# Optimization experiments

Measured on AMD Instinct MI355X. Metric: run time of the kernel, lower is better.

Reference implementation:

```python
import jax, jax.numpy as jnp
import numpy as np

B, S, H, D = 4, 4096, 8, 128
EPS = 1e-6


def layernorm(x, g, b, axes):
    m = jnp.mean(x, axis=axes, keepdims=True)
    v = jnp.mean(jnp.square(x - m), axis=axes, keepdims=True)
    return (x - m) / jnp.sqrt(v + EPS) * g + b


def setup_inputs() -> dict:
    key = jax.random.key(0)
    ks = jax.random.split(key, 6)
    scale = 0.05
    return {
        "heads_input": jax.random.normal(ks[0], (B, S, H, D), jnp.float32),
        # GroupLinear trans_hid: per-head (2D -> 3D)
        "W_hid": jax.random.normal(ks[1], (H, 2 * D, 3 * D), jnp.float32) * scale,
        "b_hid": jax.random.normal(ks[2], (H, 3 * D), jnp.float32) * scale,
        # GroupLinear trans_og: per-head (2D -> D)
        "W_og": jax.random.normal(ks[3], (H, 2 * D, D), jnp.float32) * scale,
        "b_og": jax.random.normal(ks[4], (H, D), jnp.float32) * scale,
        # LayerNorm affine params (elementwise_affine=True)
        "ln_csum_g": jnp.ones((H, D), jnp.float32),
        "ln_csum_b": jnp.zeros((H, D), jnp.float32),
        "ln_hid_g": jnp.ones((H, 3, D), jnp.float32),
        "ln_hid_b": jnp.zeros((H, 3, D), jnp.float32),
        "ln_og_g": jnp.ones((H, D), jnp.float32),
        "ln_og_b": jnp.zeros((H, D), jnp.float32),
        "init_cx": jnp.zeros((1, H, D), jnp.float32),
    }


def reference(heads_input, W_hid, b_hid, W_og, b_og, ln_csum_g, ln_csum_b,
              ln_hid_g, ln_hid_b, ln_og_g, ln_og_b, init_cx):
    b, s, h, d = heads_input.shape
    # shifted cumulative sum over time, then LayerNorm over (head, dim)
    shifted = jnp.concatenate(
        [jnp.zeros((b, 1, h, d), heads_input.dtype), heads_input[:, :-1]], axis=1)
    csum = layernorm(jnp.cumsum(shifted, axis=1), ln_csum_g, ln_csum_b, (-2, -1))
    cat = jnp.concatenate([heads_input, csum], axis=-1)        # [b,s,h,2d]
    hid = jnp.einsum('bshi,hio->bsho', cat, W_hid) + b_hid     # [b,s,h,3d]
    hid = layernorm(hid.reshape(b, s, h, 3, d), ln_hid_g, ln_hid_b, (-3, -2, -1))
    igate, fgate, hidden = hid[..., 0, :], hid[..., 1, :], hid[..., 2, :]
    fgate = jax.nn.sigmoid(fgate)
    igh = jax.nn.sigmoid(igate) * jax.nn.relu(hidden)
    # LGateFunc: cell_t = fgate_t * cell_{t-1} + igh_t, cell_0 = init_cx
    c0 = jnp.broadcast_to(init_cx, (b, h, d)).astype(heads_input.dtype)
    def step(c, fi):
        f, i = fi
        c = f * c + i
        return c, c
    _, cells = jax.lax.scan(step, c0,
                            (fgate.transpose(1, 0, 2, 3), igh.transpose(1, 0, 2, 3)))
    cell = cells.transpose(1, 0, 2, 3)                          # [b,s,h,d]
    og_in = jnp.concatenate([heads_input, cell], axis=-1)       # [b,s,h,2d]
    og = layernorm(jnp.einsum('bshi,hio->bsho', og_in, W_og) + b_og,
                   ln_og_g, ln_og_b, (-2, -1))
    return jax.nn.sigmoid(og) * cell
```

## Files before the change

kernel.cpp:

```cpp
#include <hip/hip_runtime.h>

#define EPSF 1e-6f


typedef __attribute__((ext_vector_type(8))) short short8v;
typedef __attribute__((ext_vector_type(4))) float float4v;

__device__ __forceinline__ float sigm(float x) { return 1.0f / (1.0f + __expf(-x)); }

__device__ __forceinline__ unsigned short f2bf(float f) {
    unsigned int u = __float_as_uint(f);
    u = (u + 0x7fffu + ((u >> 16) & 1u)) >> 16;
    return (unsigned short)u;
}
__device__ __forceinline__ float bf2f(unsigned short s) { return __uint_as_float(((unsigned int)s) << 16); }
__device__ __forceinline__ float bf2f_lo(unsigned int p) { return __uint_as_float(p << 16); }
__device__ __forceinline__ float bf2f_hi(unsigned int p) { return __uint_as_float(p & 0xffff0000u); }
__device__ __forceinline__ unsigned int pack2bf(float a, float b) {
    return (unsigned int)f2bf(a) | ((unsigned int)f2bf(b) << 16);
}

__device__ __forceinline__ void block_reduce2(float& a, float& b) {
#pragma unroll
    for (int off = 32; off > 0; off >>= 1) {
        a += __shfl_down(a, off);
        b += __shfl_down(b, off);
    }
    __shared__ float sa[8], sb[8];
    int wid = threadIdx.x >> 6;
    int lane = threadIdx.x & 63;
    if (lane == 0) { sa[wid] = a; sb[wid] = b; }
    __syncthreads();
    a = sa[0] + sa[1] + sa[2] + sa[3];
    b = sb[0] + sb[1] + sb[2] + sb[3];
}

__global__ __launch_bounds__(256) void k_prep_w(const float* __restrict__ Wh, const float* __restrict__ Wo,
                                                unsigned short* __restrict__ WTH,
                                                unsigned short* __restrict__ WTO) {
    int idx = blockIdx.x * 256 + threadIdx.x;
    if (idx < 786432) {
        int k = idx & 255;
        int rest = idx >> 8;
        int o = rest % 384;
        int h = rest / 384;
        WTH[idx] = f2bf(Wh[((size_t)h * 256 + k) * 384 + o]);
    } else {
        int i2 = idx - 786432;
        int k = i2 & 255;
        int rest = i2 >> 8;
        int o = rest & 127;
        int h = rest >> 7;
        WTO[i2] = f2bf(Wo[((size_t)h * 256 + k) * 128 + o]);
    }
}

__global__ __launch_bounds__(256) void k_cumsum_a(const float* __restrict__ X, float* __restrict__ cS,
                                                  unsigned short* __restrict__ XB) {
    int t = blockIdx.x * 256 + threadIdx.x;
    int d = t & 127, h = (t >> 7) & 7, k = (t >> 10) & 63, b = t >> 16;
    size_t xbase = (((size_t)(b * 4096 + k * 64)) * 8 + h) * 128 + d;
    size_t pbase = ((size_t)h * 16384 + b * 4096 + k * 64) * 128 + d;
    float s = 0.f;
    for (int j = 0; j < 64; ++j) {
        unsigned short xb = f2bf(X[xbase + (size_t)j * 1024]);
        XB[pbase + (size_t)j * 128] = xb;
        s += bf2f(xb);
    }
    cS[(size_t)((b * 8 + h) * 128 + d) * 64 + k] = s;
}

__global__ __launch_bounds__(256) void k_cumsum_b(const float* __restrict__ cS, float* __restrict__ cO) {
    int wave = (blockIdx.x * 256 + threadIdx.x) >> 6;
    int lane = threadIdx.x & 63;
    size_t idx = (size_t)wave * 64 + lane;
    float v = cS[idx];
    float incl = v;
#pragma unroll
    for (int d = 1; d < 64; d <<= 1) {
        float t = __shfl_up(incl, d);
        if (lane >= d) incl += t;
    }
    cO[idx] = incl - v;
}

__global__ __launch_bounds__(256) void k_cumsum_c(const unsigned short* __restrict__ XB,
                                                  const float* __restrict__ cO,
                                                  unsigned short* __restrict__ CSUMB) {
    int t = blockIdx.x * 256 + threadIdx.x;
    int d = t & 127, h = (t >> 7) & 7, k = (t >> 10) & 63, b = t >> 16;
    int ch = (b * 8 + h) * 128 + d;
    float run = cO[(size_t)ch * 64 + k];
    size_t pbase = ((size_t)h * 16384 + b * 4096 + k * 64) * 128 + d;
    for (int j = 0; j < 64; ++j) {
        float x = bf2f(XB[pbase + (size_t)j * 128]);
        CSUMB[pbase + (size_t)j * 128] = f2bf(run);
        run += x;
    }
}

__global__ __launch_bounds__(256) void k_ln_csum(const unsigned short* __restrict__ CSUMB,
                                                 unsigned short* __restrict__ CSB,
                                                 const float* __restrict__ g, const float* __restrict__ bb) {
    int bs = blockIdx.x, t = threadIdx.x;
    int h = t >> 5, c = t & 31;
    size_t u2i = ((size_t)h * 16384 + bs) * 32 + c;
    uint2 u = ((const uint2*)CSUMB)[u2i];
    float4 v;
    v.x = bf2f_lo(u.x); v.y = bf2f_hi(u.x);
    v.z = bf2f_lo(u.y); v.w = bf2f_hi(u.y);
    float s = v.x + v.y + v.z + v.w;
    float ss = v.x * v.x + v.y * v.y + v.z * v.z + v.w * v.w;
    block_reduce2(s, ss);
    float m = s * (1.f / 1024.f);
    float var = ss * (1.f / 1024.f) - m * m;
    float r = rsqrtf(fmaxf(var, 0.f) + EPSF);
    float4 gv = ((const float4*)g)[t];
    float4 bv = ((const float4*)bb)[t];
    uint2 o;
    o.x = pack2bf((v.x - m) * r * gv.x + bv.x, (v.y - m) * r * gv.y + bv.y);
    o.y = pack2bf((v.z - m) * r * gv.z + bv.z, (v.w - m) * r * gv.w + bv.w);
    ((uint2*)CSB)[u2i] = o;
}

__global__ __launch_bounds__(512) void k_gemm_bf16(const unsigned short* __restrict__ A1,
                                                   const unsigned short* __restrict__ A2,
                                                   const unsigned short* __restrict__ Wt,
                                                   const float* __restrict__ bias,
                                                   unsigned short* __restrict__ OUT, int Nw, int m0,
                                                   int nbx) {
    __shared__ short As[2][8192];
    __shared__ short Bs[2][8192];
    int bid = blockIdx.x;
    int h = bid & 7;
    int rest = bid >> 3;
    int bx = rest % nbx;
    int by = rest / nbx;
    int t0 = threadIdx.x;
    int lane = t0 & 63, wid = t0 >> 6;
    int wr = wid >> 1, wc = wid & 1;
    int l15 = lane & 15, l4 = lane >> 4;
    int lr = lane >> 3, lc = lane & 7;
    const int bxc = bx * 128;
    const size_t mbase = (size_t)(m0 + by * 128);
    const size_t aplane = (size_t)h * 16384;

    float4v acc[2][4];
#pragma unroll
    for (int i = 0; i < 2; ++i)
#pragma unroll
        for (int j = 0; j < 4; ++j) acc[i][j] = (float4v)(0.f);

    auto STAGE = [&](int t, int buf) {
        const unsigned short* src = (t < 2) ? A1 : A2;
        int kofs = (t & 1) * 64;
#pragma unroll
        for (int it = 0; it < 2; ++it) {
            int r0 = wid * 16 + it * 8;
            int r = r0 + lr;
            int c = lc ^ (r & 7);
            size_t g = (aplane + mbase + r) * 128 + kofs + c * 8;
            __builtin_amdgcn_global_load_lds((const __attribute__((address_space(1))) void*)(src + g),
                                             (__attribute__((address_space(3))) void*)(&As[buf][r0 * 64]),
                                             16, 0, 0);
        }
#pragma unroll
        for (int it = 0; it < 2; ++it) {
            int n0 = wid * 16 + it * 8;
            int cl = n0 + lr;
            int c = lc ^ (cl & 7);
            size_t g = ((size_t)(h * Nw + bxc + cl)) * 256 + t * 64 + c * 8;
            __builtin_amdgcn_global_load_lds((const __attribute__((address_space(1))) void*)(Wt + g),
                                             (__attribute__((address_space(3))) void*)(&Bs[buf][n0 * 64]),
                                             16, 0, 0);
        }
    };

    STAGE(0, 0);
#pragma unroll
    for (int t = 0; t < 4; ++t) {
        int cur = t & 1;
        if (t < 3) {
            STAGE(t + 1, cur ^ 1);
            asm volatile("s_waitcnt vmcnt(4)" ::: "memory");
        } else {
            asm volatile("s_waitcnt vmcnt(0)" ::: "memory");
        }
        __builtin_amdgcn_s_barrier();
        __builtin_amdgcn_sched_barrier(0);
#pragma unroll
        for (int kk = 0; kk < 2; ++kk) {
            short8v a[2], b[4];
#pragma unroll
            for (int i = 0; i < 2; ++i) {
                int r = wr * 32 + i * 16 + l15;
                int slot = (kk * 4 + l4) ^ (r & 7);
                a[i] = *(const short8v*)(&As[cur][r * 64 + slot * 8]);
            }
#pragma unroll
            for (int j = 0; j < 4; ++j) {
                int c = wc * 64 + j * 16 + l15;
                int slot = (kk * 4 + l4) ^ (c & 7);
                b[j] = *(const short8v*)(&Bs[cur][c * 64 + slot * 8]);
            }
#pragma unroll
            for (int i = 0; i < 2; ++i)
#pragma unroll
                for (int j = 0; j < 4; ++j)
                    acc[i][j] = __builtin_amdgcn_mfma_f32_16x16x32_bf16(a[i], b[j], acc[i][j], 0, 0, 0);
        }
        __builtin_amdgcn_sched_barrier(0);
        __builtin_amdgcn_s_barrier();
    }
#pragma unroll
    for (int j = 0; j < 4; ++j) {
        int o = bxc + wc * 64 + j * 16 + l15;
        float bv = bias[h * Nw + o];
#pragma unroll
        for (int i = 0; i < 2; ++i) {
            int mlb = by * 128 + wr * 32 + i * 16 + l4 * 4;
#pragma unroll
            for (int q = 0; q < 4; ++q) {
                OUT[((size_t)(mlb + q) * 8 + h) * Nw + o] = f2bf(acc[i][j][q] + bv);
            }
        }
    }
}

__global__ __launch_bounds__(256) void k_ln_gates(const unsigned short* __restrict__ HID,
                                                  unsigned short* __restrict__ FG,
                                                  unsigned short* __restrict__ IG,
                                                  const float* __restrict__ g, const float* __restrict__ bb,
                                                  int m0) {
    __shared__ float sm[3072];
    int bsl = blockIdx.x, t = threadIdx.x;
    int bs = m0 + bsl;
    const uint4* row = (const uint4*)(HID + (size_t)bsl * 3072);
    float s = 0.f, ss = 0.f;
    for (int idx = t; idx < 384; idx += 256) {
        uint4 u = row[idx];
        float f0 = bf2f_lo(u.x), f1 = bf2f_hi(u.x);
        float f2 = bf2f_lo(u.y), f3 = bf2f_hi(u.y);
        float f4 = bf2f_lo(u.z), f5 = bf2f_hi(u.z);
        float f6 = bf2f_lo(u.w), f7 = bf2f_hi(u.w);
        float* p = sm + idx * 8;
        p[0] = f0; p[1] = f1; p[2] = f2; p[3] = f3; p[4] = f4; p[5] = f5; p[6] = f6; p[7] = f7;
        s += f0 + f1 + f2 + f3 + f4 + f5 + f6 + f7;
        ss += f0 * f0 + f1 * f1 + f2 * f2 + f3 * f3 + f4 * f4 + f5 * f5 + f6 * f6 + f7 * f7;
    }
    block_reduce2(s, ss);
    float m = s * (1.f / 3072.f);
    float var = ss * (1.f / 3072.f) - m * m;
    float r = rsqrtf(fmaxf(var, 0.f) + EPSF);
    int u0 = t * 4;
    int h = u0 >> 7;
    int d0 = u0 & 127;
    float fr[4], ir[4];
#pragma unroll
    for (int q = 0; q < 4; ++q) {
        int d = d0 + q;
        float yi = sm[h * 384 + d];
        float yf = sm[h * 384 + 128 + d];
        float yh = sm[h * 384 + 256 + d];
        float ni = (yi - m) * r * g[(h * 3 + 0) * 128 + d] + bb[(h * 3 + 0) * 128 + d];
        float nf = (yf - m) * r * g[(h * 3 + 1) * 128 + d] + bb[(h * 3 + 1) * 128 + d];
        float nh = (yh - m) * r * g[(h * 3 + 2) * 128 + d] + bb[(h * 3 + 2) * 128 + d];
        fr[q] = sigm(nf);
        ir[q] = sigm(ni) * fmaxf(nh, 0.f);
    }
    uint2 fo, io;
    fo.x = pack2bf(fr[0], fr[1]); fo.y = pack2bf(fr[2], fr[3]);
    io.x = pack2bf(ir[0], ir[1]); io.y = pack2bf(ir[2], ir[3]);
    ((uint2*)(FG + (size_t)bs * 1024))[t] = fo;
    ((uint2*)(IG + (size_t)bs * 1024))[t] = io;
}

__global__ __launch_bounds__(256) void k_scan_a(const unsigned short* __restrict__ FG,
                                                const unsigned short* __restrict__ IG,
                                                float* __restrict__ cF, float* __restrict__ cC) {
    int t = blockIdx.x * 256 + threadIdx.x;
    int d2 = t & 63, h = (t >> 6) & 7, k = (t >> 9) & 63, b = t >> 15;
    size_t base = (((size_t)(b * 4096 + k * 64)) * 8 + h) * 64 + d2;
    const unsigned int* FGu = (const unsigned int*)FG;
    const unsigned int* IGu = (const unsigned int*)IG;
    float F0 = 1.f, C0 = 0.f, F1 = 1.f, C1 = 0.f;
    for (int j = 0; j < 64; ++j) {
        unsigned int fg = FGu[base + (size_t)j * 512];
        unsigned int ig = IGu[base + (size_t)j * 512];
        float f0 = bf2f_lo(fg), f1 = bf2f_hi(fg);
        C0 = fmaf(f0, C0, bf2f_lo(ig)); F0 *= f0;
        C1 = fmaf(f1, C1, bf2f_hi(ig)); F1 *= f1;
    }
    size_t ci0 = ((size_t)((b * 8 + h) * 128 + d2 * 2)) * 64 + k;
    cF[ci0] = F0; cC[ci0] = C0;
    cF[ci0 + 64] = F1; cC[ci0 + 64] = C1;
}

__global__ __launch_bounds__(256) void k_scan_b(const float* __restrict__ cF, const float* __restrict__ cC,
                                                const float* __restrict__ initcx, float* __restrict__ cI) {
    int wave = (blockIdx.x * 256 + threadIdx.x) >> 6;
    int lane = threadIdx.x & 63;
    size_t idx = (size_t)wave * 64 + lane;
    float F = cF[idx], C = cC[idx];
#pragma unroll
    for (int d = 1; d < 64; d <<= 1) {
        float Fp = __shfl_up(F, d);
        float Cp = __shfl_up(C, d);
        if (lane >= d) { C = fmaf(Cp, F, C); F *= Fp; }
    }
    float Fe = __shfl_up(F, 1);
    float Ce = __shfl_up(C, 1);
    if (lane == 0) { Fe = 1.f; Ce = 0.f; }
    float c0 = initcx[wave & 1023];
    cI[idx] = fmaf(Fe, c0, Ce);
}

__global__ __launch_bounds__(256) void k_scan_c(const unsigned short* __restrict__ FG,
                                                const unsigned short* __restrict__ IG,
                                                unsigned short* __restrict__ CLB,
                                                const float* __restrict__ cI) {
    int t = blockIdx.x * 256 + threadIdx.x;
    int d2 = t & 63, h = (t >> 6) & 7, k = (t >> 9) & 63, b = t >> 15;
    size_t base = (((size_t)(b * 4096 + k * 64)) * 8 + h) * 64 + d2;
    size_t pbase = ((size_t)h * 16384 + b * 4096 + k * 64) * 64 + d2;
    const unsigned int* FGu = (const unsigned int*)FG;
    const unsigned int* IGu = (const unsigned int*)IG;
    unsigned int* CLu = (unsigned int*)CLB;
    size_t ci0 = ((size_t)((b * 8 + h) * 128 + d2 * 2)) * 64 + k;
    float c0 = cI[ci0], c1 = cI[ci0 + 64];
    for (int j = 0; j < 64; ++j) {
        unsigned int fg = FGu[base + (size_t)j * 512];
        unsigned int ig = IGu[base + (size_t)j * 512];
        c0 = fmaf(bf2f_lo(fg), c0, bf2f_lo(ig));
        c1 = fmaf(bf2f_hi(fg), c1, bf2f_hi(ig));
        CLu[pbase + (size_t)j * 64] = pack2bf(c0, c1);
    }
}

__global__ __launch_bounds__(256) void k_ln_out(const unsigned short* __restrict__ OG,
                                                const unsigned short* __restrict__ CLB,
                                                const float* __restrict__ g, const float* __restrict__ bb,
                                                float* __restrict__ OUT, int m0) {
    int bsl = blockIdx.x, t = threadIdx.x;
    int bs = m0 + bsl;
    uint2 u = ((const uint2*)(OG + (size_t)bsl * 1024))[t];
    float4 v;
    v.x = bf2f_lo(u.x); v.y = bf2f_hi(u.x);
    v.z = bf2f_lo(u.y); v.w = bf2f_hi(u.y);
    float s = v.x + v.y + v.z + v.w;
    float ss = v.x * v.x + v.y * v.y + v.z * v.z + v.w * v.w;
    block_reduce2(s, ss);
    float m = s * (1.f / 1024.f);
    float var = ss * (1.f / 1024.f) - m * m;
    float r = rsqrtf(fmaxf(var, 0.f) + EPSF);
    float4 gv = ((const float4*)g)[t];
    float4 bv = ((const float4*)bb)[t];
    int h = t >> 5, c = t & 31;
    uint2 cu = ((const uint2*)CLB)[((size_t)h * 16384 + bs) * 32 + c];
    float4 cv;
    cv.x = bf2f_lo(cu.x); cv.y = bf2f_hi(cu.x);
    cv.z = bf2f_lo(cu.y); cv.w = bf2f_hi(cu.y);
    float4 o;
    o.x = sigm((v.x - m) * r * gv.x + bv.x) * cv.x;
    o.y = sigm((v.y - m) * r * gv.y + bv.y) * cv.y;
    o.z = sigm((v.z - m) * r * gv.z + bv.z) * cv.z;
    o.w = sigm((v.w - m) * r * gv.w + bv.w) * cv.w;
    ((float4*)(OUT + (size_t)bs * 1024))[t] = o;
}

extern "C" void kernel_launch(void* const* d_in, const int* in_sizes, int n_in,
                              void* d_out, int out_size, void* d_ws, size_t ws_size,
                              hipStream_t stream) {
    const float* X      = (const float*)d_in[0];
    const float* W_hid  = (const float*)d_in[1];
    const float* b_hid  = (const float*)d_in[2];
    const float* W_og   = (const float*)d_in[3];
    const float* b_og   = (const float*)d_in[4];
    const float* g_cs   = (const float*)d_in[5];
    const float* b_cs   = (const float*)d_in[6];
    const float* g_hid  = (const float*)d_in[7];
    const float* b_hidl = (const float*)d_in[8];
    const float* g_og   = (const float*)d_in[9];
    const float* b_ogl  = (const float*)d_in[10];
    const float* initcx = (const float*)d_in[11];

    float* ws = (float*)d_ws;
    const size_t O_SC    = 0ull;
    const size_t O_XB    = 1310720ull;
    const size_t O_CSUMB = 9699328ull;
    const size_t O_CSB   = 18087936ull;
    const size_t O_IGB   = 26476544ull;
    const size_t O_CLB   = 34865152ull;
    const size_t O_WTH   = 43253760ull;
    const size_t O_WTO   = 43646976ull;
    const size_t O_HID   = 43778048ull;

    float* cS = ws + O_SC;
    float* cO = cS + 262144;
    float* cF = cO + 262144;
    float* cC = cF + 262144;
    float* cI = cC + 262144;
    unsigned short* XB    = (unsigned short*)(ws + O_XB);
    unsigned short* CSUMB = (unsigned short*)(ws + O_CSUMB);
    unsigned short* FGB   = CSUMB;
    unsigned short* CSB   = (unsigned short*)(ws + O_CSB);
    unsigned short* IGB   = (unsigned short*)(ws + O_IGB);
    unsigned short* CLB   = (unsigned short*)(ws + O_CLB);
    unsigned short* WTH   = (unsigned short*)(ws + O_WTH);
    unsigned short* WTO   = (unsigned short*)(ws + O_WTO);
    unsigned short* HIDC  = (unsigned short*)(ws + O_HID);

    size_t avail = (ws_size / 4 > O_HID) ? ws_size / 4 - O_HID : 0;
    int CH = 1024;
    for (int c = 16384; c >= 1024; c >>= 1) {
        if ((size_t)c * 1536ull <= avail) { CH = c; break; }
    }
    const int NC = 16384 / CH;

    dim3 blk(256);
    dim3 blkg(512);
    k_prep_w<<<4096, blk, 0, stream>>>(W_hid, W_og, WTH, WTO);
    k_cumsum_a<<<1024, blk, 0, stream>>>(X, cS, XB);
    k_cumsum_b<<<1024, blk, 0, stream>>>(cS, cO);
    k_cumsum_c<<<1024, blk, 0, stream>>>(XB, cO, CSUMB);
    k_ln_csum<<<16384, blk, 0, stream>>>(CSUMB, CSB, g_cs, b_cs);
    for (int c = 0; c < NC; ++c) {
        int m0 = c * CH;
        k_gemm_bf16<<<8 * 3 * (CH / 128), blkg, 0, stream>>>(XB, CSB, WTH, b_hid, HIDC, 384, m0, 3);
        k_ln_gates<<<CH, blk, 0, stream>>>(HIDC, FGB, IGB, g_hid, b_hidl, m0);
    }
    k_scan_a<<<512, blk, 0, stream>>>(FGB, IGB, cF, cC);
    k_scan_b<<<1024, blk, 0, stream>>>(cF, cC, initcx, cI);
    k_scan_c<<<512, blk, 0, stream>>>(FGB, IGB, CLB, cI);
    for (int c = 0; c < NC; ++c) {
        int m0 = c * CH;
        k_gemm_bf16<<<8 * 1 * (CH / 128), blkg, 0, stream>>>(XB, CLB, WTO, b_og, HIDC, 128, m0, 1);
        k_ln_out<<<CH, blk, 0, stream>>>(HIDC, CLB, g_og, b_ogl, (float*)d_out, m0);
    }
}
```

Measured before the change: 237.6 us.

## Fuse gate LayerNorm with first phase of chunked cell scan

Merges the gate LayerNorm/sigmoid kernel with the per-chunk scan reduction kernel. Each block now walks 64 consecutive timesteps, writes the gates as before, and accumulates the chunk's forget-product and cell carry in registers. This removes the separate pass that re-read the forget and input gate arrays for the chunk reduction. In exchange, the grid shrinks 64x and each block runs a serial loop with a block reduction and barrier per row, which costs parallelism and latency hiding.

```diff
diff --git a/kernel.cpp b/kernel.cpp
--- a/kernel.cpp
+++ b/kernel.cpp
@@ -227,73 +227,75 @@
     }
 }
 
-__global__ __launch_bounds__(256) void k_ln_gates(const unsigned short* __restrict__ HID,
-                                                  unsigned short* __restrict__ FG,
-                                                  unsigned short* __restrict__ IG,
-                                                  const float* __restrict__ g, const float* __restrict__ bb,
-                                                  int m0) {
+__global__ __launch_bounds__(256) void k_ln_gates_scan(const unsigned short* __restrict__ HID,
+                                                       unsigned short* __restrict__ FG,
+                                                       unsigned short* __restrict__ IG,
+                                                       float* __restrict__ cF, float* __restrict__ cC,
+                                                       const float* __restrict__ g,
+                                                       const float* __restrict__ bb, int m0) {
     __shared__ float sm[3072];
-    int bsl = blockIdx.x, t = threadIdx.x;
-    int bs = m0 + bsl;
-    const uint4* row = (const uint4*)(HID + (size_t)bsl * 3072);
-    float s = 0.f, ss = 0.f;
-    for (int idx = t; idx < 384; idx += 256) {
-        uint4 u = row[idx];
-        float f0 = bf2f_lo(u.x), f1 = bf2f_hi(u.x);
-        float f2 = bf2f_lo(u.y), f3 = bf2f_hi(u.y);
-        float f4 = bf2f_lo(u.z), f5 = bf2f_hi(u.z);
-        float f6 = bf2f_lo(u.w), f7 = bf2f_hi(u.w);
-        float* p = sm + idx * 8;
-        p[0] = f0; p[1] = f1; p[2] = f2; p[3] = f3; p[4] = f4; p[5] = f5; p[6] = f6; p[7] = f7;
-        s += f0 + f1 + f2 + f3 + f4 + f5 + f6 + f7;
-        ss += f0 * f0 + f1 * f1 + f2 * f2 + f3 * f3 + f4 * f4 + f5 * f5 + f6 * f6 + f7 * f7;
-    }
-    block_reduce2(s, ss);
-    float m = s * (1.f / 3072.f);
-    float var = ss * (1.f / 3072.f) - m * m;
-    float r = rsqrtf(fmaxf(var, 0.f) + EPSF);
+    int t = threadIdx.x;
+    int bs0 = m0 + blockIdx.x * 64;
+    int b = bs0 >> 12;
+    int kch = (bs0 & 4095) >> 6;
     int u0 = t * 4;
     int h = u0 >> 7;
     int d0 = u0 & 127;
-    float fr[4], ir[4];
+    float F[4] = {1.f, 1.f, 1.f, 1.f};
+    float C[4] = {0.f, 0.f, 0.f, 0.f};
+
+    for (int j = 0; j < 64; ++j) {
+        int bs = bs0 + j;
+        int bsl = bs - m0;
+        const uint4* row = (const uint4*)(HID + (size_t)bsl * 3072);
+        float s = 0.f, ss = 0.f;
+        for (int idx = t; idx < 384; idx += 256) {
+            uint4 u = row[idx];
+            float f0 = bf2f_lo(u.x), f1 = bf2f_hi(u.x);
+            float f2 = bf2f_lo(u.y), f3 = bf2f_hi(u.y);
+            float f4 = bf2f_lo(u.z), f5 = bf2f_hi(u.z);
+            float f6 = bf2f_lo(u.w), f7 = bf2f_hi(u.w);
+            float* p = sm + idx * 8;
+            p[0] = f0; p[1] = f1; p[2] = f2; p[3] = f3; p[4] = f4; p[5] = f5; p[6] = f6; p[7] = f7;
+            s += f0 + f1 + f2 + f3 + f4 + f5 + f6 + f7;
+            ss += f0 * f0 + f1 * f1 + f2 * f2 + f3 * f3 + f4 * f4 + f5 * f5 + f6 * f6 + f7 * f7;
+        }
+        block_reduce2(s, ss);
+        float m = s * (1.f / 3072.f);
+        float var = ss * (1.f / 3072.f) - m * m;
+        float r = rsqrtf(fmaxf(var, 0.f) + EPSF);
+        float fr[4], ir[4];
+#pragma unroll
+        for (int q = 0; q < 4; ++q) {
+            int d = d0 + q;
+            float yi = sm[h * 384 + d];
+            float yf = sm[h * 384 + 128 + d];
+            float yh = sm[h * 384 + 256 + d];
+            float ni = (yi - m) * r * g[(h * 3 + 0) * 128 + d] + bb[(h * 3 + 0) * 128 + d];
+            float nf = (yf - m) * r * g[(h * 3 + 1) * 128 + d] + bb[(h * 3 + 1) * 128 + d];
+            float nh = (yh - m) * r * g[(h * 3 + 2) * 128 + d] + bb[(h * 3 + 2) * 128 + d];
+            fr[q] = sigm(nf);
+            ir[q] = sigm(ni) * fmaxf(nh, 0.f);
+        }
+        uint2 fo, io;
+        fo.x = pack2bf(fr[0], fr[1]); fo.y = pack2bf(fr[2], fr[3]);
+        io.x = pack2bf(ir[0], ir[1]); io.y = pack2bf(ir[2], ir[3]);
+        ((uint2*)(FG + (size_t)bs * 1024))[t] = fo;
+        ((uint2*)(IG + (size_t)bs * 1024))[t] = io;
+        float fq0 = bf2f_lo(fo.x), fq1 = bf2f_hi(fo.x), fq2 = bf2f_lo(fo.y), fq3 = bf2f_hi(fo.y);
+        float iq0 = bf2f_lo(io.x), iq1 = bf2f_hi(io.x), iq2 = bf2f_lo(io.y), iq3 = bf2f_hi(io.y);
+        C[0] = fmaf(fq0, C[0], iq0); F[0] *= fq0;
+        C[1] = fmaf(fq1, C[1], iq1); F[1] *= fq1;
+        C[2] = fmaf(fq2, C[2], iq2); F[2] *= fq2;
+        C[3] = fmaf(fq3, C[3], iq3); F[3] *= fq3;
+        __syncthreads();
+    }
 #pragma unroll
     for (int q = 0; q < 4; ++q) {
-        int d = d0 + q;
-        float yi = sm[h * 384 + d];
-        float yf = sm[h * 384 + 128 + d];
-        float yh = sm[h * 384 + 256 + d];
-        float ni = (yi - m) * r * g[(h * 3 + 0) * 128 + d] + bb[(h * 3 + 0) * 128 + d];
-        float nf = (yf - m) * r * g[(h * 3 + 1) * 128 + d] + bb[(h * 3 + 1) * 128 + d];
-        float nh = (yh - m) * r * g[(h * 3 + 2) * 128 + d] + bb[(h * 3 + 2) * 128 + d];
-        fr[q] = sigm(nf);
-        ir[q] = sigm(ni) * fmaxf(nh, 0.f);
-    }
-    uint2 fo, io;
-    fo.x = pack2bf(fr[0], fr[1]); fo.y = pack2bf(fr[2], fr[3]);
-    io.x = pack2bf(ir[0], ir[1]); io.y = pack2bf(ir[2], ir[3]);
-    ((uint2*)(FG + (size_t)bs * 1024))[t] = fo;
-    ((uint2*)(IG + (size_t)bs * 1024))[t] = io;
-}
-
-__global__ __launch_bounds__(256) void k_scan_a(const unsigned short* __restrict__ FG,
-                                                const unsigned short* __restrict__ IG,
-                                                float* __restrict__ cF, float* __restrict__ cC) {
-    int t = blockIdx.x * 256 + threadIdx.x;
-    int d2 = t & 63, h = (t >> 6) & 7, k = (t >> 9) & 63, b = t >> 15;
-    size_t base = (((size_t)(b * 4096 + k * 64)) * 8 + h) * 64 + d2;
-    const unsigned int* FGu = (const unsigned int*)FG;
-    const unsigned int* IGu = (const unsigned int*)IG;
-    float F0 = 1.f, C0 = 0.f, F1 = 1.f, C1 = 0.f;
-    for (int j = 0; j < 64; ++j) {
-        unsigned int fg = FGu[base + (size_t)j * 512];
-        unsigned int ig = IGu[base + (size_t)j * 512];
-        float f0 = bf2f_lo(fg), f1 = bf2f_hi(fg);
-        C0 = fmaf(f0, C0, bf2f_lo(ig)); F0 *= f0;
-        C1 = fmaf(f1, C1, bf2f_hi(ig)); F1 *= f1;
-    }
-    size_t ci0 = ((size_t)((b * 8 + h) * 128 + d2 * 2)) * 64 + k;
-    cF[ci0] = F0; cC[ci0] = C0;
-    cF[ci0 + 64] = F1; cC[ci0 + 64] = C1;
+        size_t ci = ((size_t)((b * 8 + h) * 128 + d0 + q)) * 64 + kch;
+        cF[ci] = F[q];
+        cC[ci] = C[q];
+    }
 }
 
 __global__ __launch_bounds__(256) void k_scan_b(const float* __restrict__ cF, const float* __restrict__ cC,
@@ -427,9 +429,8 @@
     for (int c = 0; c < NC; ++c) {
         int m0 = c * CH;
         k_gemm_bf16<<<8 * 3 * (CH / 128), blkg, 0, stream>>>(XB, CSB, WTH, b_hid, HIDC, 384, m0, 3);
-        k_ln_gates<<<CH, blk, 0, stream>>>(HIDC, FGB, IGB, g_hid, b_hidl, m0);
-    }
-    k_scan_a<<<512, blk, 0, stream>>>(FGB, IGB, cF, cC);
+        k_ln_gates_scan<<<CH / 64, blk, 0, stream>>>(HIDC, FGB, IGB, cF, cC, g_hid, b_hidl, m0);
+    }
     k_scan_b<<<1024, blk, 0, stream>>>(cF, cC, initcx, cI);
     k_scan_c<<<512, blk, 0, stream>>>(FGB, IGB, CLB, cI);
     for (int c = 0; c < NC; ++c) {
```

Measured after the change: 376.3 us. 1.58x slower.
